# Kernel tuning notes

Measured on AMD Instinct MI355X. Metric: run time of the kernel, lower is better.

Reference implementation:

```python
import jax, jax.numpy as jnp
import numpy as np

B, TK, H = 32, 8192, 256

def setup_inputs() -> dict:
    key = jax.random.key(0)
    ks = jax.random.split(key, 10)
    s = 0.02
    return {
        "s_t_hat": jax.random.normal(ks[0], (B, 2 * H), dtype=jnp.float32),
        "encoder_outputs": jax.random.normal(ks[1], (B, TK, H), dtype=jnp.float32),
        "enc_padding_mask": jnp.ones((B, TK), dtype=jnp.float32),
        "coverage": jax.random.uniform(ks[2], (B, TK), dtype=jnp.float32),
        "attn_dist_node_to_token": jax.random.uniform(ks[3], (B, TK), dtype=jnp.float32),
        "We": jax.random.normal(ks[4], (H, H), dtype=jnp.float32) * s,   # encode_proj weight
        "Wd": jax.random.normal(ks[5], (H, 2 * H), dtype=jnp.float32) * s,  # decode_proj weight
        "bd": jax.random.normal(ks[6], (H,), dtype=jnp.float32) * s,     # decode_proj bias
        "wc": jax.random.normal(ks[7], (H,), dtype=jnp.float32) * s,     # W_c weight (Linear(1,H))
        "v": jax.random.normal(ks[8], (H,), dtype=jnp.float32) * s,      # v weight (Linear(H,1))
    }

def reference(s_t_hat, encoder_outputs, enc_padding_mask, coverage,
              attn_dist_node_to_token, We, Wd, bd, wc, v):
    # encoder projection: [b,t,h] @ We^T -> [b,t,h]
    enc_feat = jnp.einsum('bth,gh->btg', encoder_outputs, We)
    # decoder projection: [b,2h] @ Wd^T + bd -> [b,h]
    dec_fea = s_t_hat @ Wd.T + bd
    # coverage feature: outer product coverage[b,t] x wc[h]
    att_features = enc_feat + dec_fea[:, None, :] + coverage[..., None] * wc
    e = jnp.tanh(att_features)
    scores = jnp.einsum('bth,h->bt', e, v)  # [b, t_k]
    attn_ = jax.nn.softmax(scores, axis=1) * enc_padding_mask
    attn = attn_ / jnp.sum(attn_, axis=1, keepdims=True)
    c_t = jnp.einsum('bt,bth->bh', attn, encoder_outputs)  # context
    new_cov = jnp.clip(coverage + attn, 0.0, 1.0)
    return (c_t, attn, new_cov)
```

## Files before the change

### kernel.cpp

```cpp
#include <hip/hip_runtime.h>

#define B_  32
#define TK_ 8192
#define H_  256
#define MT  64

typedef __bf16 bf16_t;
typedef __bf16 bf16x4 __attribute__((ext_vector_type(4)));
typedef __bf16 bf16x8 __attribute__((ext_vector_type(8)));
typedef float  floatx4 __attribute__((ext_vector_type(4)));

__device__ __forceinline__ float tanh_fast(float x) {
    float e = __builtin_amdgcn_exp2f(x * 2.885390081777927f);
    return 1.0f - 2.0f * __builtin_amdgcn_rcpf(e + 1.0f);
}

__global__ void prep_kernel(const float* __restrict__ s_t_hat,
                            const float* __restrict__ We,
                            const float* __restrict__ Wd,
                            const float* __restrict__ bd,
                            bf16_t* __restrict__ We_bf,
                            float* __restrict__ dec_ws,
                            float* __restrict__ D_ws) {
    int tid = threadIdx.x, blk = blockIdx.x;
    int gid = blk * 256 + tid;
    We_bf[gid] = (bf16_t)We[gid];

    if (gid < 32) D_ws[gid] = 0.f;

    if (blk >= 32 && blk < 160) {
        int idx  = (blk - 32) * 256 + tid;
        int pair = idx >> 2, q = idx & 3;
        int b = pair >> 8, i = pair & 255;
        const float4* sp = (const float4*)(s_t_hat + b * 2 * H_ + q * 128);
        const float4* wp = (const float4*)(Wd + (size_t)i * 2 * H_ + q * 128);
        float sum = 0.f;
        #pragma unroll 8
        for (int ii = 0; ii < 32; ++ii) {
            float4 a = sp[ii], w = wp[ii];
            sum += a.x * w.x + a.y * w.y + a.z * w.z + a.w * w.w;
        }
        sum += __shfl_xor(sum, 1, 64);
        sum += __shfl_xor(sum, 2, 64);
        if (q == 0) dec_ws[pair] = sum + bd[i];
    }
}

__global__ __launch_bounds__(256, 4) void attn_main(
    const float* __restrict__ enc,
    const float* __restrict__ mask,
    const float* __restrict__ cov,
    const float* __restrict__ wc,
    const float* __restrict__ v,
    const bf16_t* __restrict__ We_bf,
    const float* __restrict__ dec_ws,
    float* __restrict__ ctx_part,
    float* __restrict__ D_ws,
    float* __restrict__ attn_out) {

    __shared__ __align__(16) bf16_t As[MT * 264];
    __shared__ float dec_s[256], wc_s[256], v_s[256];
    __shared__ float cov_s[64], mask_s[64], wexp[64];
    __shared__ float sp[4][64];

    const int tid  = threadIdx.x;
    const int b    = blockIdx.y;
    const int t0   = blockIdx.x * MT;
    const int lane = tid & 63, w = tid >> 6;
    const int l15  = lane & 15, l4 = lane >> 4;

    dec_s[tid] = dec_ws[b * 256 + tid];
    wc_s[tid]  = wc[tid];
    v_s[tid]   = v[tid];
    if (tid < 64)       cov_s[tid]       = cov[(size_t)b * TK_ + t0 + tid];
    else if (tid < 128) mask_s[tid - 64] = mask[(size_t)b * TK_ + t0 + tid - 64];

    const float* encb = enc + ((size_t)b * TK_ + t0) * H_;
    const int h4 = lane * 4;
    {
        float4 r[8];
        #pragma unroll
        for (int it = 0; it < 8; ++it)
            r[it] = *(const float4*)(encb + (size_t)(it * 4 + w) * H_ + h4);
        #pragma unroll
        for (int it = 0; it < 8; ++it) {
            bf16x4 p;
            p[0] = (bf16_t)r[it].x; p[1] = (bf16_t)r[it].y;
            p[2] = (bf16_t)r[it].z; p[3] = (bf16_t)r[it].w;
            *(bf16x4*)(&As[(it * 4 + w) * 264 + h4]) = p;
        }
        #pragma unroll
        for (int it = 0; it < 8; ++it)
            r[it] = *(const float4*)(encb + (size_t)((it + 8) * 4 + w) * H_ + h4);
        #pragma unroll
        for (int it = 0; it < 8; ++it) {
            bf16x4 p;
            p[0] = (bf16_t)r[it].x; p[1] = (bf16_t)r[it].y;
            p[2] = (bf16_t)r[it].z; p[3] = (bf16_t)r[it].w;
            *(bf16x4*)(&As[((it + 8) * 4 + w) * 264 + h4]) = p;
        }
    }
    __syncthreads();

    floatx4 acc[4][4];
    #pragma unroll
    for (int mi = 0; mi < 4; ++mi)
        #pragma unroll
        for (int ni = 0; ni < 4; ++ni)
            acc[mi][ni] = (floatx4){0.f, 0.f, 0.f, 0.f};

    const int wbase = w * 64;
    const bf16_t* Bp = We_bf + (size_t)wbase * 256;
    const int kf = l4 * 8;

    bf16x8 bq[4];
    #pragma unroll
    for (int ni = 0; ni < 4; ++ni)
        bq[ni] = *(const bf16x8*)(Bp + (size_t)(ni * 16 + l15) * 256 + kf);

    #pragma unroll
    for (int ks = 0; ks < 8; ++ks) {
        bf16x8 bqn[4];
        if (ks < 7) {
            int kn = (ks + 1) * 32 + kf;
            #pragma unroll
            for (int ni = 0; ni < 4; ++ni)
                bqn[ni] = *(const bf16x8*)(Bp + (size_t)(ni * 16 + l15) * 256 + kn);
        }
        int k = ks * 32 + kf;
        bf16x8 a[4];
        #pragma unroll
        for (int mi = 0; mi < 4; ++mi)
            a[mi] = *(const bf16x8*)(&As[(mi * 16 + l15) * 264 + k]);
        #pragma unroll
        for (int mi = 0; mi < 4; ++mi)
            #pragma unroll
            for (int ni = 0; ni < 4; ++ni)
                acc[mi][ni] = __builtin_amdgcn_mfma_f32_16x16x32_bf16(
                    a[mi], bq[ni], acc[mi][ni], 0, 0, 0);
        if (ks < 7) {
            #pragma unroll
            for (int ni = 0; ni < 4; ++ni)
                bq[ni] = bqn[ni];
        }
    }

    float decv[4], wcv[4], vv[4];
    #pragma unroll
    for (int ni = 0; ni < 4; ++ni) {
        int g = wbase + ni * 16 + l15;
        decv[ni] = dec_s[g]; wcv[ni] = wc_s[g]; vv[ni] = v_s[g];
    }
    #pragma unroll
    for (int mi = 0; mi < 4; ++mi) {
        #pragma unroll
        for (int r = 0; r < 4; ++r) {
            int t = mi * 16 + l4 * 4 + r;
            float cv = cov_s[t];
            float s = 0.f;
            #pragma unroll
            for (int ni = 0; ni < 4; ++ni) {
                float af = acc[mi][ni][r] + decv[ni] + cv * wcv[ni];
                s += tanh_fast(af) * vv[ni];
            }
            s += __shfl_xor(s, 1, 64);
            s += __shfl_xor(s, 2, 64);
            s += __shfl_xor(s, 4, 64);
            s += __shfl_xor(s, 8, 64);
            if (l15 == 0) sp[w][t] = s;
        }
    }
    __syncthreads();

    if (tid < 64) {
        int t = tid;
        float sc = sp[0][t] + sp[1][t] + sp[2][t] + sp[3][t];
        float wv = __builtin_amdgcn_exp2f(sc * 1.4426950408889634f) * mask_s[t];
        wexp[t] = wv;
        attn_out[(size_t)b * TK_ + t0 + t] = wv;
        float d = wv;
        d += __shfl_xor(d, 1, 64);  d += __shfl_xor(d, 2, 64);
        d += __shfl_xor(d, 4, 64);  d += __shfl_xor(d, 8, 64);
        d += __shfl_xor(d, 16, 64); d += __shfl_xor(d, 32, 64);
        if (tid == 0) atomicAdd(&D_ws[b], d);
    }
    dec_s[tid] = 0.f;
    __syncthreads();

    {
        int h0 = lane * 4;
        float c0 = 0, c1 = 0, c2 = 0, c3 = 0;
        #pragma unroll
        for (int tt = 0; tt < 16; ++tt) {
            int t = w * 16 + tt;
            float wv = wexp[t];
            bf16x4 q = *(const bf16x4*)(&As[t * 264 + h0]);
            c0 += wv * (float)q[0];
            c1 += wv * (float)q[1];
            c2 += wv * (float)q[2];
            c3 += wv * (float)q[3];
        }
        atomicAdd(&dec_s[h0 + 0], c0);
        atomicAdd(&dec_s[h0 + 1], c1);
        atomicAdd(&dec_s[h0 + 2], c2);
        atomicAdd(&dec_s[h0 + 3], c3);
    }
    __syncthreads();
    ctx_part[((size_t)b * 128 + blockIdx.x) * 256 + tid] = dec_s[tid];
}

__global__ void finalize_kernel(const float* __restrict__ cov,
                                const float* __restrict__ ctx_part,
                                const float* __restrict__ D_ws,
                                float* __restrict__ out) {
    int b = blockIdx.y, chunk = blockIdx.x, tid = threadIdx.x;
    float invD = 1.0f / D_ws[b];
    int idx = chunk * 256 + tid;
    size_t gi = (size_t)b * TK_ + idx;
    float* attn = out + 8192;
    float* ncov = out + 8192 + (size_t)B_ * TK_;
    float a = attn[gi] * invD;
    attn[gi] = a;
    float nc = cov[gi] + a;
    ncov[gi] = fminf(fmaxf(nc, 0.f), 1.f);
    if (chunk == 0) {
        const float* p = ctx_part + (size_t)b * 128 * 256 + tid;
        float s0 = 0, s1 = 0, s2 = 0, s3 = 0;
        #pragma unroll 4
        for (int j = 0; j < 128; j += 4) {
            s0 += p[(j + 0) * 256];
            s1 += p[(j + 1) * 256];
            s2 += p[(j + 2) * 256];
            s3 += p[(j + 3) * 256];
        }
        out[b * 256 + tid] = ((s0 + s1) + (s2 + s3)) * invD;
    }
}

extern "C" void kernel_launch(void* const* d_in, const int* in_sizes, int n_in,
                              void* d_out, int out_size, void* d_ws, size_t ws_size,
                              hipStream_t stream) {
    const float* s_t_hat = (const float*)d_in[0];
    const float* enc     = (const float*)d_in[1];
    const float* mask    = (const float*)d_in[2];
    const float* cov     = (const float*)d_in[3];
    const float* We      = (const float*)d_in[5];
    const float* Wd      = (const float*)d_in[6];
    const float* bd      = (const float*)d_in[7];
    const float* wc      = (const float*)d_in[8];
    const float* v       = (const float*)d_in[9];
    float* out = (float*)d_out;

    char* ws = (char*)d_ws;
    bf16_t* We_bf  = (bf16_t*)ws;
    float*  dec_ws = (float*)(ws + 131072);
    float*  D_ws   = (float*)(ws + 131072 + 32768);
    float*  ctx_part = (float*)(ws + 131072 + 32768 + 256);

    prep_kernel<<<256, 256, 0, stream>>>(s_t_hat, We, Wd, bd, We_bf, dec_ws, D_ws);
    attn_main<<<dim3(128, 32), 256, 0, stream>>>(enc, mask, cov, wc, v, We_bf,
                                                 dec_ws, ctx_part, D_ws, out + 8192);
    finalize_kernel<<<dim3(32, 32), 256, 0, stream>>>(cov, ctx_part, D_ws, out);
}
```

Before: 454.4 us.

## Process four token tiles per block in a loop and accumulate context in LDS

The attention kernel now loops over four 64-token tiles per block, shrinking the grid from 128x32 to 32x32 blocks. The context and denominator partials are accumulated in shared memory and registers across tiles, so each block does one global atomic and writes a quarter as many ctx partials. The exp weights are broadcast with wave shuffles instead of an LDS array. This lowers launch and partial-reduction overhead but leaves only 1024 blocks, and the serial tile loop has no overlap between the global loads of one tile and the compute of the previous, which may reduce latency hiding.

```diff
diff --git a/kernel.cpp b/kernel.cpp
--- a/kernel.cpp
+++ b/kernel.cpp
@@ -4,6 +4,7 @@
 #define TK_ 8192
 #define H_  256
 #define MT  64
+#define NT  4
 
 typedef __bf16 bf16_t;
 typedef __bf16 bf16x4 __attribute__((ext_vector_type(4)));
@@ -60,153 +61,158 @@
 
     __shared__ __align__(16) bf16_t As[MT * 264];
     __shared__ float dec_s[256], wc_s[256], v_s[256];
-    __shared__ float cov_s[64], mask_s[64], wexp[64];
+    __shared__ float cov_s[64], mask_s[64];
     __shared__ float sp[4][64];
+    __shared__ float ctx_acc[256];
 
     const int tid  = threadIdx.x;
     const int b    = blockIdx.y;
-    const int t0   = blockIdx.x * MT;
     const int lane = tid & 63, w = tid >> 6;
     const int l15  = lane & 15, l4 = lane >> 4;
+    const int h4   = lane * 4;
+    const int wbase = w * 64;
+    const int kf = l4 * 8;
+    const bf16_t* Bp = We_bf + (size_t)wbase * 256;
 
     dec_s[tid] = dec_ws[b * 256 + tid];
     wc_s[tid]  = wc[tid];
     v_s[tid]   = v[tid];
-    if (tid < 64)       cov_s[tid]       = cov[(size_t)b * TK_ + t0 + tid];
-    else if (tid < 128) mask_s[tid - 64] = mask[(size_t)b * TK_ + t0 + tid - 64];
-
-    const float* encb = enc + ((size_t)b * TK_ + t0) * H_;
-    const int h4 = lane * 4;
-    {
-        float4 r[8];
-        #pragma unroll
-        for (int it = 0; it < 8; ++it)
-            r[it] = *(const float4*)(encb + (size_t)(it * 4 + w) * H_ + h4);
-        #pragma unroll
-        for (int it = 0; it < 8; ++it) {
-            bf16x4 p;
-            p[0] = (bf16_t)r[it].x; p[1] = (bf16_t)r[it].y;
-            p[2] = (bf16_t)r[it].z; p[3] = (bf16_t)r[it].w;
-            *(bf16x4*)(&As[(it * 4 + w) * 264 + h4]) = p;
-        }
-        #pragma unroll
-        for (int it = 0; it < 8; ++it)
-            r[it] = *(const float4*)(encb + (size_t)((it + 8) * 4 + w) * H_ + h4);
-        #pragma unroll
-        for (int it = 0; it < 8; ++it) {
-            bf16x4 p;
-            p[0] = (bf16_t)r[it].x; p[1] = (bf16_t)r[it].y;
-            p[2] = (bf16_t)r[it].z; p[3] = (bf16_t)r[it].w;
-            *(bf16x4*)(&As[((it + 8) * 4 + w) * 264 + h4]) = p;
-        }
+    ctx_acc[tid] = 0.f;
+
+    float dsum = 0.f;
+
+    for (int it4 = 0; it4 < NT; ++it4) {
+        const int t0 = (blockIdx.x * NT + it4) * MT;
+
+        if (tid < 64)       cov_s[tid]       = cov[(size_t)b * TK_ + t0 + tid];
+        else if (tid < 128) mask_s[tid - 64] = mask[(size_t)b * TK_ + t0 + tid - 64];
+
+        const float* encb = enc + ((size_t)b * TK_ + t0) * H_;
+        {
+            float4 r[8];
+            #pragma unroll
+            for (int it = 0; it < 8; ++it)
+                r[it] = *(const float4*)(encb + (size_t)(it * 4 + w) * H_ + h4);
+            #pragma unroll
+            for (int it = 0; it < 8; ++it) {
+                bf16x4 p;
+                p[0] = (bf16_t)r[it].x; p[1] = (bf16_t)r[it].y;
+                p[2] = (bf16_t)r[it].z; p[3] = (bf16_t)r[it].w;
+                *(bf16x4*)(&As[(it * 4 + w) * 264 + h4]) = p;
+            }
+            #pragma unroll
+            for (int it = 0; it < 8; ++it)
+                r[it] = *(const float4*)(encb + (size_t)((it + 8) * 4 + w) * H_ + h4);
+            #pragma unroll
+            for (int it = 0; it < 8; ++it) {
+                bf16x4 p;
+                p[0] = (bf16_t)r[it].x; p[1] = (bf16_t)r[it].y;
+                p[2] = (bf16_t)r[it].z; p[3] = (bf16_t)r[it].w;
+                *(bf16x4*)(&As[((it + 8) * 4 + w) * 264 + h4]) = p;
+            }
+        }
+        __syncthreads();
+
+        floatx4 acc[4][4];
+        #pragma unroll
+        for (int mi = 0; mi < 4; ++mi)
+            #pragma unroll
+            for (int ni = 0; ni < 4; ++ni)
+                acc[mi][ni] = (floatx4){0.f, 0.f, 0.f, 0.f};
+
+        bf16x8 bq[4];
+        #pragma unroll
+        for (int ni = 0; ni < 4; ++ni)
+            bq[ni] = *(const bf16x8*)(Bp + (size_t)(ni * 16 + l15) * 256 + kf);
+
+        #pragma unroll
+        for (int ks = 0; ks < 8; ++ks) {
+            bf16x8 bqn[4];
+            if (ks < 7) {
+                int kn = (ks + 1) * 32 + kf;
+                #pragma unroll
+                for (int ni = 0; ni < 4; ++ni)
+                    bqn[ni] = *(const bf16x8*)(Bp + (size_t)(ni * 16 + l15) * 256 + kn);
+            }
+            int k = ks * 32 + kf;
+            bf16x8 a[4];
+            #pragma unroll
+            for (int mi = 0; mi < 4; ++mi)
+                a[mi] = *(const bf16x8*)(&As[(mi * 16 + l15) * 264 + k]);
+            #pragma unroll
+            for (int mi = 0; mi < 4; ++mi)
+                #pragma unroll
+                for (int ni = 0; ni < 4; ++ni)
+                    acc[mi][ni] = __builtin_amdgcn_mfma_f32_16x16x32_bf16(
+                        a[mi], bq[ni], acc[mi][ni], 0, 0, 0);
+            if (ks < 7) {
+                #pragma unroll
+                for (int ni = 0; ni < 4; ++ni)
+                    bq[ni] = bqn[ni];
+            }
+        }
+
+        float decv[4], wcv[4], vv[4];
+        #pragma unroll
+        for (int ni = 0; ni < 4; ++ni) {
+            int g = wbase + ni * 16 + l15;
+            decv[ni] = dec_s[g]; wcv[ni] = wc_s[g]; vv[ni] = v_s[g];
+        }
+        #pragma unroll
+        for (int mi = 0; mi < 4; ++mi) {
+            #pragma unroll
+            for (int r = 0; r < 4; ++r) {
+                int t = mi * 16 + l4 * 4 + r;
+                float cv = cov_s[t];
+                float s = 0.f;
+                #pragma unroll
+                for (int ni = 0; ni < 4; ++ni) {
+                    float af = acc[mi][ni][r] + decv[ni] + cv * wcv[ni];
+                    s += tanh_fast(af) * vv[ni];
+                }
+                s += __shfl_xor(s, 1, 64);
+                s += __shfl_xor(s, 2, 64);
+                s += __shfl_xor(s, 4, 64);
+                s += __shfl_xor(s, 8, 64);
+                if (l15 == 0) sp[w][t] = s;
+            }
+        }
+        __syncthreads();
+
+        float sc = sp[0][lane] + sp[1][lane] + sp[2][lane] + sp[3][lane];
+        float wv = __builtin_amdgcn_exp2f(sc * 1.4426950408889634f) * mask_s[lane];
+
+        if (w == 0) {
+            attn_out[(size_t)b * TK_ + t0 + lane] = wv;
+            float d = wv;
+            d += __shfl_xor(d, 1, 64);  d += __shfl_xor(d, 2, 64);
+            d += __shfl_xor(d, 4, 64);  d += __shfl_xor(d, 8, 64);
+            d += __shfl_xor(d, 16, 64); d += __shfl_xor(d, 32, 64);
+            dsum += d;
+        }
+
+        {
+            float c0 = 0, c1 = 0, c2 = 0, c3 = 0;
+            #pragma unroll
+            for (int tt = 0; tt < 16; ++tt) {
+                int t = w * 16 + tt;
+                float wvt = __shfl(wv, t, 64);
+                bf16x4 q = *(const bf16x4*)(&As[t * 264 + h4]);
+                c0 += wvt * (float)q[0];
+                c1 += wvt * (float)q[1];
+                c2 += wvt * (float)q[2];
+                c3 += wvt * (float)q[3];
+            }
+            atomicAdd(&ctx_acc[h4 + 0], c0);
+            atomicAdd(&ctx_acc[h4 + 1], c1);
+            atomicAdd(&ctx_acc[h4 + 2], c2);
+            atomicAdd(&ctx_acc[h4 + 3], c3);
+        }
+        __syncthreads();
     }
-    __syncthreads();
-
-    floatx4 acc[4][4];
-    #pragma unroll
-    for (int mi = 0; mi < 4; ++mi)
-        #pragma unroll
-        for (int ni = 0; ni < 4; ++ni)
-            acc[mi][ni] = (floatx4){0.f, 0.f, 0.f, 0.f};
-
-    const int wbase = w * 64;
-    const bf16_t* Bp = We_bf + (size_t)wbase * 256;
-    const int kf = l4 * 8;
-
-    bf16x8 bq[4];
-    #pragma unroll
-    for (int ni = 0; ni < 4; ++ni)
-        bq[ni] = *(const bf16x8*)(Bp + (size_t)(ni * 16 + l15) * 256 + kf);
-
-    #pragma unroll
-    for (int ks = 0; ks < 8; ++ks) {
-        bf16x8 bqn[4];
-        if (ks < 7) {
-            int kn = (ks + 1) * 32 + kf;
-            #pragma unroll
-            for (int ni = 0; ni < 4; ++ni)
-                bqn[ni] = *(const bf16x8*)(Bp + (size_t)(ni * 16 + l15) * 256 + kn);
-        }
-        int k = ks * 32 + kf;
-        bf16x8 a[4];
-        #pragma unroll
-        for (int mi = 0; mi < 4; ++mi)
-            a[mi] = *(const bf16x8*)(&As[(mi * 16 + l15) * 264 + k]);
-        #pragma unroll
-        for (int mi = 0; mi < 4; ++mi)
-            #pragma unroll
-            for (int ni = 0; ni < 4; ++ni)
-                acc[mi][ni] = __builtin_amdgcn_mfma_f32_16x16x32_bf16(
-                    a[mi], bq[ni], acc[mi][ni], 0, 0, 0);
-        if (ks < 7) {
-            #pragma unroll
-            for (int ni = 0; ni < 4; ++ni)
-                bq[ni] = bqn[ni];
-        }
-    }
-
-    float decv[4], wcv[4], vv[4];
-    #pragma unroll
-    for (int ni = 0; ni < 4; ++ni) {
-        int g = wbase + ni * 16 + l15;
-        decv[ni] = dec_s[g]; wcv[ni] = wc_s[g]; vv[ni] = v_s[g];
-    }
-    #pragma unroll
-    for (int mi = 0; mi < 4; ++mi) {
-        #pragma unroll
-        for (int r = 0; r < 4; ++r) {
-            int t = mi * 16 + l4 * 4 + r;
-            float cv = cov_s[t];
-            float s = 0.f;
-            #pragma unroll
-            for (int ni = 0; ni < 4; ++ni) {
-                float af = acc[mi][ni][r] + decv[ni] + cv * wcv[ni];
-                s += tanh_fast(af) * vv[ni];
-            }
-            s += __shfl_xor(s, 1, 64);
-            s += __shfl_xor(s, 2, 64);
-            s += __shfl_xor(s, 4, 64);
-            s += __shfl_xor(s, 8, 64);
-            if (l15 == 0) sp[w][t] = s;
-        }
-    }
-    __syncthreads();
-
-    if (tid < 64) {
-        int t = tid;
-        float sc = sp[0][t] + sp[1][t] + sp[2][t] + sp[3][t];
-        float wv = __builtin_amdgcn_exp2f(sc * 1.4426950408889634f) * mask_s[t];
-        wexp[t] = wv;
-        attn_out[(size_t)b * TK_ + t0 + t] = wv;
-        float d = wv;
-        d += __shfl_xor(d, 1, 64);  d += __shfl_xor(d, 2, 64);
-        d += __shfl_xor(d, 4, 64);  d += __shfl_xor(d, 8, 64);
-        d += __shfl_xor(d, 16, 64); d += __shfl_xor(d, 32, 64);
-        if (tid == 0) atomicAdd(&D_ws[b], d);
-    }
-    dec_s[tid] = 0.f;
-    __syncthreads();
-
-    {
-        int h0 = lane * 4;
-        float c0 = 0, c1 = 0, c2 = 0, c3 = 0;
-        #pragma unroll
-        for (int tt = 0; tt < 16; ++tt) {
-            int t = w * 16 + tt;
-            float wv = wexp[t];
-            bf16x4 q = *(const bf16x4*)(&As[t * 264 + h0]);
-            c0 += wv * (float)q[0];
-            c1 += wv * (float)q[1];
-            c2 += wv * (float)q[2];
-            c3 += wv * (float)q[3];
-        }
-        atomicAdd(&dec_s[h0 + 0], c0);
-        atomicAdd(&dec_s[h0 + 1], c1);
-        atomicAdd(&dec_s[h0 + 2], c2);
-        atomicAdd(&dec_s[h0 + 3], c3);
-    }
-    __syncthreads();
-    ctx_part[((size_t)b * 128 + blockIdx.x) * 256 + tid] = dec_s[tid];
+
+    if (tid == 0) atomicAdd(&D_ws[b], dsum);
+    ctx_part[((size_t)b * 32 + blockIdx.x) * 256 + tid] = ctx_acc[tid];
 }
 
 __global__ void finalize_kernel(const float* __restrict__ cov,
@@ -224,10 +230,10 @@
     float nc = cov[gi] + a;
     ncov[gi] = fminf(fmaxf(nc, 0.f), 1.f);
     if (chunk == 0) {
-        const float* p = ctx_part + (size_t)b * 128 * 256 + tid;
+        const float* p = ctx_part + (size_t)b * 32 * 256 + tid;
         float s0 = 0, s1 = 0, s2 = 0, s3 = 0;
-        #pragma unroll 4
-        for (int j = 0; j < 128; j += 4) {
+        #pragma unroll
+        for (int j = 0; j < 32; j += 4) {
             s0 += p[(j + 0) * 256];
             s1 += p[(j + 1) * 256];
             s2 += p[(j + 2) * 256];
@@ -255,10 +261,10 @@
     bf16_t* We_bf  = (bf16_t*)ws;
     float*  dec_ws = (float*)(ws + 131072);
     float*  D_ws   = (float*)(ws + 131072 + 32768);
-    float*  ctx_part = (float*)(ws + 131072 + 32768 + 256);
+    float*  ctx_part = (float*)(ws + 196608);
 
     prep_kernel<<<256, 256, 0, stream>>>(s_t_hat, We, Wd, bd, We_bf, dec_ws, D_ws);
-    attn_main<<<dim3(128, 32), 256, 0, stream>>>(enc, mask, cov, wc, v, We_bf,
-                                                 dec_ws, ctx_part, D_ws, out + 8192);
+    attn_main<<<dim3(32, 32), 256, 0, stream>>>(enc, mask, cov, wc, v, We_bf,
+                                                dec_ws, ctx_part, D_ws, out + 8192);
     finalize_kernel<<<dim3(32, 32), 256, 0, stream>>>(cov, ctx_part, D_ws, out);
 }
```

After: 499.7 us. +10.0%, slower.
